# Kernel tuning notes

Measured on AMD Instinct MI355X. Metric: run time of the kernel, lower is better.

## Reference

```python
import jax, jax.numpy as jnp
import numpy as np

MAX_NEIGHBORS = 64  # static cap; >> observed max (~50) for n=9225 uniform pts, r=0.03


def setup_inputs() -> dict:
    key = jax.random.key(0)
    k1, k2 = jax.random.split(key)
    n_batch, n, m, d = 8, 9225, 4096, 2
    data = jax.random.uniform(k1, (n_batch, n, d), dtype=jnp.float32)
    queries = jax.random.uniform(k2, (n_batch, m, d), dtype=jnp.float32)
    radius = jnp.float32(0.03)
    return {"data": data, "queries": queries, "radius": radius}


def reference(data, queries, radius):
    # Faithful JAX translation of native_neighbor_search (use_open3d=False),
    # computed in one shot instead of q_chunk loops (same math), with a static
    # neighbor cap MAX_NEIGHBORS standing in for the data-dependent max.
    B, n, d = data.shape
    m = queries.shape[1]
    # Squared Euclidean distances via the GEMM expansion (equiv. to cdist<=r).
    qn = jnp.sum(queries * queries, axis=-1)              # [B, m]
    dn = jnp.sum(data * data, axis=-1)                    # [B, n]
    cross = jnp.einsum("bmd,bnd->bmn", queries, data)    # [B, m, n]
    sqd = jnp.maximum(qn[:, :, None] + dn[:, None, :] - 2.0 * cross, 0.0)
    in_nbr = sqd <= radius * radius                       # [B, m, n] bool
    counts = jnp.sum(in_nbr, axis=2).astype(jnp.int32)    # [B, m]
    idx = jnp.arange(n, dtype=jnp.int32)                  # [n]
    # invalid slots -> sentinel n, sort compacts valid indices to the front
    valid = jnp.where(in_nbr, idx[None, None, :], jnp.int32(n))
    sorted_idx = jnp.sort(valid, axis=2)[:, :, :MAX_NEIGHBORS]
    neighbors_index = jnp.where(sorted_idx == n, jnp.int32(-1), sorted_idx)
    neighbors_row_splits = jnp.concatenate(
        [jnp.zeros((B, 1), dtype=jnp.int32), jnp.cumsum(counts, axis=1)], axis=1
    )
    return neighbors_index, neighbors_row_splits
```

## Files before the change

kernel.cpp:

```cpp
#include <hip/hip_runtime.h>

#define BATCH 8
#define NPTS 9225
#define MQ 4096
#define CAP 64
#define GRID 32
#define NCELLS (GRID * GRID)

__device__ __forceinline__ int cell_of(float x, float y) {
  int cx = (int)(x * (float)GRID);
  int cy = (int)(y * (float)GRID);
  cx = min(max(cx, 0), GRID - 1);
  cy = min(max(cy, 0), GRID - 1);
  return cy * GRID + cx;
}

__global__ __launch_bounds__(1024) void build_kernel(
    const float* __restrict__ data,
    int* __restrict__ cell_starts,
    float2* __restrict__ sdata, int* __restrict__ sidx) {
  __shared__ int hist[NCELLS];
  __shared__ int cursor[NCELLS];
  const int b = blockIdx.x;
  const int t = threadIdx.x;
  hist[t] = 0;
  __syncthreads();

  const float2* dp = (const float2*)data + (size_t)b * NPTS;
  float2 pts[10];
  int cells[10];
  int np = 0;
  for (int i = t; i < NPTS; i += 1024) {
    const float2 p = dp[i];
    const int c = cell_of(p.x, p.y);
    pts[np] = p;
    cells[np] = c;
    ++np;
    atomicAdd(&hist[c], 1);
  }
  __syncthreads();

  const int v = hist[t];
  for (int off = 1; off < NCELLS; off <<= 1) {
    const int u = (t >= off) ? hist[t - off] : 0;
    __syncthreads();
    hist[t] += u;
    __syncthreads();
  }
  const int incl = hist[t];
  const int excl = incl - v;
  cursor[t] = excl;
  cell_starts[b * (NCELLS + 1) + t] = excl;
  if (t == NCELLS - 1) cell_starts[b * (NCELLS + 1) + NCELLS] = incl;
  __syncthreads();

  float2* sd = sdata + (size_t)b * NPTS;
  int* si = sidx + (size_t)b * NPTS;
  for (int k = 0; k < np; ++k) {
    const int pos = atomicAdd(&cursor[cells[k]], 1);
    sd[pos] = pts[k];
    si[pos] = t + k * 1024;
  }
}

__global__ __launch_bounds__(256) void search_kernel(
    const float* __restrict__ queries, const float* __restrict__ radius_p,
    const int* __restrict__ cell_starts, const float2* __restrict__ sdata,
    const int* __restrict__ sidx, int* __restrict__ nbr_idx,
    int* __restrict__ counts) {
#pragma clang fp contract(off)
  __shared__ int hitbuf[4][CAP];
  const int wave_g = (blockIdx.x * blockDim.x + threadIdx.x) >> 6;
  const int lane = threadIdx.x & 63;
  const int w = (threadIdx.x >> 6) & 3;
  if (wave_g >= BATCH * MQ) return;
  const int q = wave_g;
  const int b = q >> 12;
  const float r = radius_p[0];
  const float r2 = r * r;
  const float2 qv = ((const float2*)queries)[q];
  const float qx = qv.x, qy = qv.y;
  const float qn = qx * qx + qy * qy;

  const int cx = min(max((int)(qx * (float)GRID), 0), GRID - 1);
  const int cy = min(max((int)(qy * (float)GRID), 0), GRID - 1);
  const int x0 = max(cx - 1, 0), x1 = min(cx + 1, GRID - 1);
  const int y0 = max(cy - 1, 0), y1 = min(cy + 1, GRID - 1);

  const int csbase = b * (NCELLS + 1);
  int rstart[3], rlen[3];
  int nr = 0;
  for (int y = y0; y <= y1; ++y) {
    const int s0 = cell_starts[csbase + y * GRID + x0];
    const int s1 = cell_starts[csbase + y * GRID + x1 + 1];
    rstart[nr] = s0;
    rlen[nr] = s1 - s0;
    ++nr;
  }
  for (int k = nr; k < 3; ++k) { rstart[k] = 0; rlen[k] = 0; }
  const int L0 = rlen[0];
  const int L01 = L0 + rlen[1];
  const int T = L01 + rlen[2];

  const unsigned long long below = (1ull << lane) - 1ull;
  const float2* sd = sdata + (size_t)b * NPTS;
  const int* si = sidx + (size_t)b * NPTS;
  int h = 0;

  for (int base = 0; base < T; base += 64) {
    const int p = base + lane;
    const bool act = (p < T);
    int i;
    if (p < L0)        i = rstart[0] + p;
    else if (p < L01)  i = rstart[1] + (p - L0);
    else               i = rstart[2] + (p - L01);
    if (!act) i = 0;
    const float2 pt = sd[i];
    const int id = si[i];
    const float dx = pt.x, dy = pt.y;
    const float dn = dx * dx + dy * dy;
    const float cross = qx * dx + qy * dy;
    const float s = (qn + dn) - 2.0f * cross;
    const bool in = act && (s <= r2);
    const unsigned long long mask = __ballot(in);
    if (mask != 0ull) {
      if (in) {
        const int pos = h + __popcll(mask & below);
        if (pos < CAP) hitbuf[w][pos] = id;
      }
      h += __popcll(mask);
    }
  }

  int v = (lane < h && lane < CAP) ? hitbuf[w][lane] : 0x7fffffff;

#pragma unroll
  for (int k = 2; k <= 32; k <<= 1) {
#pragma unroll
    for (int j = k >> 1; j >= 1; j >>= 1) {
      const int other = __shfl_xor(v, j, 64);
      const bool keep_min = (((lane & k) == 0) == ((lane & j) == 0));
      v = keep_min ? min(v, other) : max(v, other);
    }
  }
  if (h > 32) {
#pragma unroll
    for (int j = 32; j >= 1; j >>= 1) {
      const int other = __shfl_xor(v, j, 64);
      const bool keep_min = ((lane & j) == 0);
      v = keep_min ? min(v, other) : max(v, other);
    }
  }

  nbr_idx[(size_t)q * CAP + lane] = (v == 0x7fffffff) ? -1 : v;
  if (lane == 0) counts[q] = h;
}

__global__ __launch_bounds__(256) void scan_kernel(const int* __restrict__ counts,
                                                   int* __restrict__ row_splits) {
  const int b = blockIdx.x;
  const int t = threadIdx.x;
  const int T = 256;
  const int PER = MQ / T;
  __shared__ int partial[T];
  const int* c = counts + b * MQ;
  int local[PER];
  int sum = 0;
#pragma unroll
  for (int k = 0; k < PER; ++k) { local[k] = c[t * PER + k]; sum += local[k]; }
  partial[t] = sum;
  __syncthreads();
  for (int off = 1; off < T; off <<= 1) {
    int u = (t >= off) ? partial[t - off] : 0;
    __syncthreads();
    partial[t] += u;
    __syncthreads();
  }
  const int excl = (t == 0) ? 0 : partial[t - 1];
  int* rs = row_splits + b * (MQ + 1);
  if (t == 0) rs[0] = 0;
  int run = excl;
#pragma unroll
  for (int k = 0; k < PER; ++k) { run += local[k]; rs[t * PER + k + 1] = run; }
}

extern "C" void kernel_launch(void* const* d_in, const int* in_sizes, int n_in,
                              void* d_out, int out_size, void* d_ws, size_t ws_size,
                              hipStream_t stream) {
  const float* data    = (const float*)d_in[0];
  const float* queries = (const float*)d_in[1];
  const float* radius  = (const float*)d_in[2];
  int* out        = (int*)d_out;
  int* nbr_idx    = out;
  int* row_splits = out + BATCH * MQ * CAP;

  int* counts      = (int*)d_ws;
  int* cell_starts = counts + BATCH * MQ;
  int* sidx        = cell_starts + BATCH * (NCELLS + 1);
  float2* sdata    = (float2*)(sidx + BATCH * NPTS);

  hipLaunchKernelGGL(build_kernel, dim3(BATCH), dim3(1024), 0, stream,
                     data, cell_starts, sdata, sidx);
  hipLaunchKernelGGL(search_kernel, dim3(BATCH * MQ / 4), dim3(256), 0, stream,
                     queries, radius, cell_starts, sdata, sidx, nbr_idx, counts);
  hipLaunchKernelGGL(scan_kernel, dim3(BATCH), dim3(256), 0, stream,
                     counts, row_splits);
}
```

Before: 102.9 us.

## Fuse row-split scan into search kernel via last-block-per-batch completion counter

```diff
diff --git a/kernel.cpp b/kernel.cpp
--- a/kernel.cpp
+++ b/kernel.cpp
@@ -18,26 +18,20 @@
 __global__ __launch_bounds__(1024) void build_kernel(
     const float* __restrict__ data,
     int* __restrict__ cell_starts,
-    float2* __restrict__ sdata, int* __restrict__ sidx) {
+    float2* __restrict__ sdata, int* __restrict__ sidx,
+    int* __restrict__ done_flags) {
   __shared__ int hist[NCELLS];
   __shared__ int cursor[NCELLS];
   const int b = blockIdx.x;
   const int t = threadIdx.x;
+  if (t == 0)
+    __hip_atomic_store(&done_flags[b], 0, __ATOMIC_RELAXED, __HIP_MEMORY_SCOPE_AGENT);
   hist[t] = 0;
   __syncthreads();
 
   const float2* dp = (const float2*)data + (size_t)b * NPTS;
-  float2 pts[10];
-  int cells[10];
-  int np = 0;
-  for (int i = t; i < NPTS; i += 1024) {
-    const float2 p = dp[i];
-    const int c = cell_of(p.x, p.y);
-    pts[np] = p;
-    cells[np] = c;
-    ++np;
-    atomicAdd(&hist[c], 1);
-  }
+  for (int i = t; i < NPTS; i += 1024)
+    atomicAdd(&hist[cell_of(dp[i].x, dp[i].y)], 1);
   __syncthreads();
 
   const int v = hist[t];
@@ -56,10 +50,11 @@
 
   float2* sd = sdata + (size_t)b * NPTS;
   int* si = sidx + (size_t)b * NPTS;
-  for (int k = 0; k < np; ++k) {
-    const int pos = atomicAdd(&cursor[cells[k]], 1);
-    sd[pos] = pts[k];
-    si[pos] = t + k * 1024;
+  for (int i = t; i < NPTS; i += 1024) {
+    const float2 p = dp[i];
+    const int pos = atomicAdd(&cursor[cell_of(p.x, p.y)], 1);
+    sd[pos] = p;
+    si[pos] = i;
   }
 }
 
@@ -67,14 +62,15 @@
     const float* __restrict__ queries, const float* __restrict__ radius_p,
     const int* __restrict__ cell_starts, const float2* __restrict__ sdata,
     const int* __restrict__ sidx, int* __restrict__ nbr_idx,
-    int* __restrict__ counts) {
+    int* __restrict__ counts, int* __restrict__ done_flags,
+    int* __restrict__ row_splits) {
 #pragma clang fp contract(off)
   __shared__ int hitbuf[4][CAP];
-  const int wave_g = (blockIdx.x * blockDim.x + threadIdx.x) >> 6;
+  __shared__ int partial[256];
+  __shared__ int lastflag;
   const int lane = threadIdx.x & 63;
-  const int w = (threadIdx.x >> 6) & 3;
-  if (wave_g >= BATCH * MQ) return;
-  const int q = wave_g;
+  const int w = threadIdx.x >> 6;
+  const int q = blockIdx.x * 4 + w;
   const int b = q >> 12;
   const float r = radius_p[0];
   const float r2 = r * r;
@@ -153,35 +149,45 @@
   }
 
   nbr_idx[(size_t)q * CAP + lane] = (v == 0x7fffffff) ? -1 : v;
-  if (lane == 0) counts[q] = h;
-}
-
-__global__ __launch_bounds__(256) void scan_kernel(const int* __restrict__ counts,
-                                                   int* __restrict__ row_splits) {
-  const int b = blockIdx.x;
-  const int t = threadIdx.x;
-  const int T = 256;
-  const int PER = MQ / T;
-  __shared__ int partial[T];
-  const int* c = counts + b * MQ;
-  int local[PER];
-  int sum = 0;
-#pragma unroll
-  for (int k = 0; k < PER; ++k) { local[k] = c[t * PER + k]; sum += local[k]; }
-  partial[t] = sum;
-  __syncthreads();
-  for (int off = 1; off < T; off <<= 1) {
-    int u = (t >= off) ? partial[t - off] : 0;
+  if (lane == 0)
+    __hip_atomic_store(&counts[q], h, __ATOMIC_RELAXED, __HIP_MEMORY_SCOPE_AGENT);
+
+  __syncthreads();
+  if (threadIdx.x == 0) {
+    __threadfence();
+    const int old = __hip_atomic_fetch_add(&done_flags[b], 1,
+                                           __ATOMIC_ACQ_REL, __HIP_MEMORY_SCOPE_AGENT);
+    lastflag = (old == (MQ / 4) - 1);
+  }
+  __syncthreads();
+  if (lastflag) {
+    __threadfence();
+    const int t = threadIdx.x;
+    const int PER = MQ / 256;
+    const int* c = counts + b * MQ;
+    int local[PER];
+    int sum = 0;
+#pragma unroll
+    for (int k = 0; k < PER; ++k) {
+      local[k] = __hip_atomic_load(&c[t * PER + k], __ATOMIC_RELAXED,
+                                   __HIP_MEMORY_SCOPE_AGENT);
+      sum += local[k];
+    }
+    partial[t] = sum;
     __syncthreads();
-    partial[t] += u;
-    __syncthreads();
-  }
-  const int excl = (t == 0) ? 0 : partial[t - 1];
-  int* rs = row_splits + b * (MQ + 1);
-  if (t == 0) rs[0] = 0;
-  int run = excl;
-#pragma unroll
-  for (int k = 0; k < PER; ++k) { run += local[k]; rs[t * PER + k + 1] = run; }
+    for (int off = 1; off < 256; off <<= 1) {
+      const int u = (t >= off) ? partial[t - off] : 0;
+      __syncthreads();
+      partial[t] += u;
+      __syncthreads();
+    }
+    const int excl = (t == 0) ? 0 : partial[t - 1];
+    int* rs = row_splits + b * (MQ + 1);
+    if (t == 0) rs[0] = 0;
+    int run = excl;
+#pragma unroll
+    for (int k = 0; k < PER; ++k) { run += local[k]; rs[t * PER + k + 1] = run; }
+  }
 }
 
 extern "C" void kernel_launch(void* const* d_in, const int* in_sizes, int n_in,
@@ -196,13 +202,13 @@
 
   int* counts      = (int*)d_ws;
   int* cell_starts = counts + BATCH * MQ;
-  int* sidx        = cell_starts + BATCH * (NCELLS + 1);
-  float2* sdata    = (float2*)(sidx + BATCH * NPTS);
+  int* done_flags  = cell_starts + BATCH * (NCELLS + 1);
+  int* sidx        = done_flags + BATCH;
+  float2* sdata    = (float2*)(sidx + BATCH * NPTS + 2);
 
   hipLaunchKernelGGL(build_kernel, dim3(BATCH), dim3(1024), 0, stream,
-                     data, cell_starts, sdata, sidx);
+                     data, cell_starts, sdata, sidx, done_flags);
   hipLaunchKernelGGL(search_kernel, dim3(BATCH * MQ / 4), dim3(256), 0, stream,
-                     queries, radius, cell_starts, sdata, sidx, nbr_idx, counts);
-  hipLaunchKernelGGL(scan_kernel, dim3(BATCH), dim3(256), 0, stream,
-                     counts, row_splits);
-}
+                     queries, radius, cell_starts, sdata, sidx, nbr_idx,
+                     counts, done_flags, row_splits);
+}
```

Result: slower. 403.7 us (+292.3%).
